# Optimization experiments

Measured on AMD Instinct MI355X. Metric: run time of the kernel, lower is better.

## Reference

```python
import jax, jax.numpy as jnp
import numpy as np
from jax import lax

TAU = 1.0
LAMBDA_CONTRAST = 1.0
GAMMA_ALIGN = 1.0
EPSILON = 0.1
SINKHORN_ITERS = 50
B, V_EN, V_CN, K, H, D = 512, 30000, 20000, 100, 512, 300


def setup_inputs() -> dict:
    key = jax.random.key(0)
    ks = jax.random.split(key, 24)
    s = lambda fan_in: 1.0 / np.sqrt(fan_in)
    inp = {
        'x_bow_en': jax.random.uniform(ks[0], (B, V_EN), jnp.float32),
        'x_bow_cn': jax.random.uniform(ks[1], (B, V_CN), jnp.float32),
        'cluster_ids': jax.random.randint(ks[2], (B,), 0, 9, jnp.int32),
        'eps_en': jax.random.normal(ks[3], (B, K), jnp.float32),
        'eps_cn': jax.random.normal(ks[4], (B, K), jnp.float32),
        # English encoder params
        'W1_en': jax.random.normal(ks[5], (V_EN, H), jnp.float32) * s(V_EN),
        'b1_en': jnp.zeros((H,), jnp.float32),
        'W2_en': jax.random.normal(ks[6], (H, H), jnp.float32) * s(H),
        'b2_en': jnp.zeros((H,), jnp.float32),
        'Wmu_en': jax.random.normal(ks[7], (H, K), jnp.float32) * s(H),
        'bmu_en': jnp.zeros((K,), jnp.float32),
        'Wlv_en': jax.random.normal(ks[8], (H, K), jnp.float32) * s(H),
        'blv_en': jnp.zeros((K,), jnp.float32),
        # Chinese encoder params
        'W1_cn': jax.random.normal(ks[9], (V_CN, H), jnp.float32) * s(V_CN),
        'b1_cn': jnp.zeros((H,), jnp.float32),
        'W2_cn': jax.random.normal(ks[10], (H, H), jnp.float32) * s(H),
        'b2_cn': jnp.zeros((H,), jnp.float32),
        'Wmu_cn': jax.random.normal(ks[11], (H, K), jnp.float32) * s(H),
        'bmu_cn': jnp.zeros((K,), jnp.float32),
        'Wlv_cn': jax.random.normal(ks[12], (H, K), jnp.float32) * s(H),
        'blv_cn': jnp.zeros((K,), jnp.float32),
        # frozen word embeddings + topic embeddings
        'word_emb_en': jax.random.normal(ks[13], (V_EN, D), jnp.float32),
        'word_emb_cn': jax.random.normal(ks[14], (V_CN, D), jnp.float32),
        'topic_emb': jax.random.normal(ks[15], (K, D), jnp.float32),
    }
    return inp


def _encoder(x, eps, W1, b1, W2, b2, Wmu, bmu, Wlv, blv):
    h = jax.nn.softplus(x @ W1 + b1)
    h = jax.nn.softplus(h @ W2 + b2)
    mu = h @ Wmu + bmu
    logvar = h @ Wlv + blv
    z = mu + eps * jnp.exp(0.5 * logvar)  # reparameterization
    theta = jax.nn.softmax(z, axis=-1)
    return theta, mu, logvar


def _compute_beta(word_emb, topic_emb, tau):
    # torch.cdist p=2 -> euclidean distance [V, K]
    sq = (jnp.sum(word_emb ** 2, -1)[:, None] + jnp.sum(topic_emb ** 2, -1)[None, :]
          - 2.0 * word_emb @ topic_emb.T)
    dist = jnp.sqrt(jnp.maximum(sq, 0.0))
    beta = jnp.exp(-dist / tau)
    beta = beta / jnp.sum(beta, axis=0, keepdims=True)  # normalize over vocab
    return beta.T  # [K, V]


def _tm_loss(x_bow, theta, beta, mu, logvar):
    recon = theta @ beta  # [B, V]
    recon_loss = jnp.mean(-jnp.sum(x_bow * jax.nn.log_softmax(recon, axis=-1), axis=-1))
    kl = jnp.mean(0.5 * jnp.sum(jnp.exp(logvar) + mu ** 2 - 1.0 - logvar, axis=-1))
    return recon_loss + kl


def _contrastive_loss(theta_en, theta_cn, cluster_ids, tau):
    b = theta_en.shape[0]
    parity = (jnp.arange(b) % 2 == 0)[:, None]
    thetas = jnp.where(parity, theta_en, theta_cn)  # anchor/other selection
    tn = thetas / jnp.maximum(jnp.linalg.norm(thetas, axis=-1, keepdims=True), 1e-8)
    E = jnp.exp((tn @ tn.T) / tau)  # exp(cos_sim / tau), [B, B]
    offdiag = ~jnp.eye(b, dtype=bool)
    valid = cluster_ids > 0  # falsy cluster -> skipped, matching torch truthiness
    same = cluster_ids[:, None] == cluster_ids[None, :]
    pos_mask = offdiag & same & valid[:, None] & valid[None, :]
    pos_sim = jnp.sum(jnp.where(pos_mask, E, 0.0), axis=1)
    neg_sum = jnp.sum(jnp.where(offdiag, E, 0.0), axis=1)  # all j != i
    has_pos = valid & (jnp.sum(pos_mask, axis=1) > 0)
    per = -jnp.log(pos_sim / (pos_sim + neg_sum + 1e-8))
    loss = jnp.sum(jnp.where(has_pos, per, 0.0))
    count = jnp.sum(has_pos).astype(jnp.float32)
    return loss / (count + 1e-8)


def _sinkhorn(a, b, C, eps):
    Kmat = jnp.exp(-C / eps)
    def step(uv, _):
        u, v = uv
        u = a / (Kmat @ v + 1e-8)
        v = b / (Kmat.T @ u + 1e-8)
        return (u, v), None
    (u, v), _ = lax.scan(step, (jnp.ones_like(a), jnp.ones_like(b)), None, length=SINKHORN_ITERS)
    return u[:, None] * Kmat * v[None, :]


def _alignment_loss(topic_emb, eps):
    tn = topic_emb / jnp.maximum(jnp.linalg.norm(topic_emb, axis=-1, keepdims=True), 1e-8)
    C = 1.0 - tn @ tn.T
    k = topic_emb.shape[0]
    a = jnp.full((k,), 1.0 / k, jnp.float32)
    Q = _sinkhorn(a, a, C, eps)
    return jnp.sum(Q * C)


def reference(x_bow_en, x_bow_cn, cluster_ids, eps_en, eps_cn,
              W1_en, b1_en, W2_en, b2_en, Wmu_en, bmu_en, Wlv_en, blv_en,
              W1_cn, b1_cn, W2_cn, b2_cn, Wmu_cn, bmu_cn, Wlv_cn, blv_cn,
              word_emb_en, word_emb_cn, topic_emb):
    theta_en, mu_en, lv_en = _encoder(x_bow_en, eps_en, W1_en, b1_en, W2_en, b2_en, Wmu_en, bmu_en, Wlv_en, blv_en)
    theta_cn, mu_cn, lv_cn = _encoder(x_bow_cn, eps_cn, W1_cn, b1_cn, W2_cn, b2_cn, Wmu_cn, bmu_cn, Wlv_cn, blv_cn)
    beta_en = _compute_beta(word_emb_en, topic_emb, TAU)
    beta_cn = _compute_beta(word_emb_cn, topic_emb, TAU)
    tm_en = _tm_loss(x_bow_en, theta_en, beta_en, mu_en, lv_en)
    tm_cn = _tm_loss(x_bow_cn, theta_cn, beta_cn, mu_cn, lv_cn)
    contrast = _contrastive_loss(theta_en, theta_cn, cluster_ids, TAU)
    align = _alignment_loss(topic_emb, EPSILON)
    total = tm_en + tm_cn + LAMBDA_CONTRAST * contrast + GAMMA_ALIGN * align
    return total, tm_en, tm_cn, contrast, align, theta_en, theta_cn, beta_en, beta_cn
```

## Files before the change

### kernel.cpp

```cpp
#include <hip/hip_runtime.h>
#include <math.h>

#define BATCH 512
#define VEN 30000
#define VCN 20000
#define KT 100
#define HID 512
#define DIM 300
#define VENP 30080
#define VCNP 20096
#define KDP 320

typedef float f32x4 __attribute__((ext_vector_type(4)));
typedef short bf16x8 __attribute__((ext_vector_type(8)));
typedef unsigned short u16x8 __attribute__((ext_vector_type(8)));
typedef unsigned short u16x4 __attribute__((ext_vector_type(4)));

#define WS_H1_EN   0
#define WS_H2_EN   (WS_H1_EN + 262144)
#define WS_H1_CN   (WS_H2_EN + 262144)
#define WS_H2_CN   (WS_H1_CN + 262144)
#define WS_ROWS_EN (WS_H2_CN + 262144)
#define WS_ROWS_CN (WS_ROWS_EN + 1536)
#define WS_SCAL    (WS_ROWS_CN + 1536)
#define ZERO_FLOATS (WS_SCAL + 64)
#define WS_BIG     ZERO_FLOATS
#define XB_EN      WS_BIG
#define XB_CN      (WS_BIG + 7680000)
#define WEP_EN     WS_BIG
#define WEP_CN     (WS_BIG + 4812800)
#define TEP        (WS_BIG + 4812800 + 3215360)
#define BT_EN      (WS_BIG + 8048640)
#define BT_CN      (BT_EN + 1925120)
#define THP_EN     (BT_CN + 1286144)
#define THP_CN     (THP_EN + 32768)
#define AFTER_BIG  (WS_BIG + 12800000)
#define W1T_EN     AFTER_BIG
#define W1T_CN     (W1T_EN + 7680000)
#define W2T_EN     (W1T_CN + 5120000)
#define W2T_CN     (W2T_EN + 131072)
#define H1B_EN     (W2T_CN + 131072)
#define H1B_CN     (H1B_EN + 131072)
#define WN2_EN     (H1B_CN + 131072)
#define WN2_CN     (WN2_EN + 30080)
#define TN2        (WN2_CN + 20096)
#define WS_TNBUF   (TN2 + 128)
#define WS_TNT     (WS_TNBUF + 51200)
#define WS_CTOP    (WS_TNT + 30000)
#define WS_COLSUM_EN (WS_CTOP + 10000)
#define WS_COLSUM_CN (WS_COLSUM_EN + 128)

#define OUT_THETA_EN 5
#define OUT_THETA_CN (OUT_THETA_EN + 51200)
#define OUT_BETA_EN  (OUT_THETA_CN + 51200)
#define OUT_BETA_CN  (OUT_BETA_EN + 3000000)

__device__ __forceinline__ float waveReduceSum(float v) {
    #pragma unroll
    for (int o = 32; o > 0; o >>= 1) v += __shfl_down(v, o);
    return v;
}

__device__ __forceinline__ unsigned short f2bf(float f) {
    unsigned int u = __float_as_uint(f);
    u = (u + 0x7FFFu + ((u >> 16) & 1u)) >> 16;
    return (unsigned short)u;
}

template <int MODE>
__global__ __launch_bounds__(256)
void mfma_gemm_nt(const unsigned short* __restrict__ A, const unsigned short* __restrict__ B,
                  float* __restrict__ C, int M, int N, int K, int ldA, int ldB, int chunkK,
                  int Mreal, const float* __restrict__ an2, const float* __restrict__ bn2)
{
    __shared__ __align__(16) unsigned short As[128 * 40];
    __shared__ __align__(16) unsigned short Bs[128 * 40];
    const int tid = threadIdx.x;
    const int m0 = blockIdx.x * 128, n0 = blockIdx.y * 128;
    const int kStart = blockIdx.z * chunkK;
    const int kEnd = min(kStart + chunkK, K);

    const int wave = tid >> 6, lane = tid & 63;
    const int wm = (wave & 1) * 64, wn = (wave >> 1) * 64;
    const int l15 = lane & 15, quad = lane >> 4;

    const int srow = tid >> 1;
    const int scol = (tid & 1) * 16;

    f32x4 acc[4][4];
    #pragma unroll
    for (int i = 0; i < 4; ++i)
        #pragma unroll
        for (int j = 0; j < 4; ++j)
            acc[i][j] = (f32x4){0.f, 0.f, 0.f, 0.f};

    const u16x8 z8 = {0,0,0,0,0,0,0,0};

    for (int k0 = kStart; k0 < kEnd; k0 += 32) {
        int kA = k0 + scol;
        {
            const unsigned short* pa = A + (size_t)(m0 + srow) * ldA + kA;
            u16x8 a0 = (kA     < kEnd) ? *(const u16x8*)(pa)     : z8;
            u16x8 a1 = (kA + 8 < kEnd) ? *(const u16x8*)(pa + 8) : z8;
            *(u16x8*)&As[srow * 40 + scol]     = a0;
            *(u16x8*)&As[srow * 40 + scol + 8] = a1;
        }
        {
            const unsigned short* pb = B + (size_t)(n0 + srow) * ldB + kA;
            u16x8 b0 = (kA     < kEnd) ? *(const u16x8*)(pb)     : z8;
            u16x8 b1 = (kA + 8 < kEnd) ? *(const u16x8*)(pb + 8) : z8;
            *(u16x8*)&Bs[srow * 40 + scol]     = b0;
            *(u16x8*)&Bs[srow * 40 + scol + 8] = b1;
        }
        __syncthreads();
        bf16x8 af[4], bfr[4];
        #pragma unroll
        for (int mi = 0; mi < 4; ++mi)
            af[mi] = *(const bf16x8*)&As[(wm + mi * 16 + l15) * 40 + quad * 8];
        #pragma unroll
        for (int ni = 0; ni < 4; ++ni)
            bfr[ni] = *(const bf16x8*)&Bs[(wn + ni * 16 + l15) * 40 + quad * 8];
        #pragma unroll
        for (int mi = 0; mi < 4; ++mi)
            #pragma unroll
            for (int ni = 0; ni < 4; ++ni)
                acc[mi][ni] = __builtin_amdgcn_mfma_f32_16x16x32_bf16(af[mi], bfr[ni], acc[mi][ni], 0, 0, 0);
        __syncthreads();
    }

    if (MODE == 0) {
        #pragma unroll
        for (int mi = 0; mi < 4; ++mi)
            #pragma unroll
            for (int ni = 0; ni < 4; ++ni)
                #pragma unroll
                for (int i = 0; i < 4; ++i) {
                    int m = m0 + wm + mi * 16 + quad * 4 + i;
                    int n = n0 + wn + ni * 16 + l15;
                    atomicAdd(&C[(size_t)m * N + n], acc[mi][ni][i]);
                }
    } else {
        #pragma unroll
        for (int mi = 0; mi < 4; ++mi)
            #pragma unroll
            for (int ni = 0; ni < 4; ++ni)
                #pragma unroll
                for (int i = 0; i < 4; ++i) {
                    int m = m0 + wm + mi * 16 + quad * 4 + i;
                    int n = n0 + wn + ni * 16 + l15;
                    if (m < Mreal && n < KT) {
                        float sq = an2[m] + bn2[n] - 2.f * acc[mi][ni][i];
                        C[(size_t)n * Mreal + m] = __expf(-sqrtf(fmaxf(sq, 0.f)));
                    }
                }
    }
}

__global__ __launch_bounds__(256)
void recon_mfma_kernel(const unsigned short* __restrict__ A, const unsigned short* __restrict__ B,
                       const float* __restrict__ x, int V, float* __restrict__ rows)
{
    __shared__ __align__(16) unsigned short As[128 * 40];
    __shared__ __align__(16) unsigned short Bs[128 * 40];
    const int tid = threadIdx.x;
    const int m0 = blockIdx.x * 128, n0 = blockIdx.y * 128;
    const int wave = tid >> 6, lane = tid & 63;
    const int wm = (wave & 1) * 64, wn = (wave >> 1) * 64;
    const int l15 = lane & 15, quad = lane >> 4;
    const int srow = tid >> 1, scol = (tid & 1) * 16;

    f32x4 acc[4][4];
    #pragma unroll
    for (int i = 0; i < 4; ++i)
        #pragma unroll
        for (int j = 0; j < 4; ++j)
            acc[i][j] = (f32x4){0.f, 0.f, 0.f, 0.f};

    for (int k0 = 0; k0 < 128; k0 += 32) {
        int kA = k0 + scol;
        *(u16x8*)&As[srow * 40 + scol]     = *(const u16x8*)(A + (size_t)(m0 + srow) * 128 + kA);
        *(u16x8*)&As[srow * 40 + scol + 8] = *(const u16x8*)(A + (size_t)(m0 + srow) * 128 + kA + 8);
        *(u16x8*)&Bs[srow * 40 + scol]     = *(const u16x8*)(B + (size_t)(n0 + srow) * 128 + kA);
        *(u16x8*)&Bs[srow * 40 + scol + 8] = *(const u16x8*)(B + (size_t)(n0 + srow) * 128 + kA + 8);
        __syncthreads();
        bf16x8 af[4], bfr[4];
        #pragma unroll
        for (int mi = 0; mi < 4; ++mi)
            af[mi] = *(const bf16x8*)&As[(wm + mi * 16 + l15) * 40 + quad * 8];
        #pragma unroll
        for (int ni = 0; ni < 4; ++ni)
            bfr[ni] = *(const bf16x8*)&Bs[(wn + ni * 16 + l15) * 40 + quad * 8];
        #pragma unroll
        for (int mi = 0; mi < 4; ++mi)
            #pragma unroll
            for (int ni = 0; ni < 4; ++ni)
                acc[mi][ni] = __builtin_amdgcn_mfma_f32_16x16x32_bf16(af[mi], bfr[ni], acc[mi][ni], 0, 0, 0);
        __syncthreads();
    }

    #pragma unroll
    for (int ni = 0; ni < 4; ++ni) {
        int b = n0 + wn + ni * 16 + l15;
        float tse = 0.f, tsxr = 0.f, tsx = 0.f;
        #pragma unroll
        for (int mi = 0; mi < 4; ++mi) {
            int v0 = m0 + wm + mi * 16 + quad * 4;
            if (v0 + 3 < V) {
                float4 xv = *(const float4*)&x[(size_t)b * V + v0];
                float xa[4] = {xv.x, xv.y, xv.z, xv.w};
                #pragma unroll
                for (int i = 0; i < 4; ++i) {
                    float r = acc[mi][ni][i];
                    tse += __expf(r);
                    tsxr += xa[i] * r;
                    tsx  += xa[i];
                }
            } else {
                #pragma unroll
                for (int i = 0; i < 4; ++i) {
                    int v = v0 + i;
                    if (v < V) {
                        float xv1 = x[(size_t)b * V + v];
                        float r = acc[mi][ni][i];
                        tse += __expf(r); tsxr += xv1 * r; tsx += xv1;
                    }
                }
            }
        }
        tse  += __shfl_xor(tse, 16);  tse  += __shfl_xor(tse, 32);
        tsxr += __shfl_xor(tsxr, 16); tsxr += __shfl_xor(tsxr, 32);
        tsx  += __shfl_xor(tsx, 16);  tsx  += __shfl_xor(tsx, 32);
        if (quad == 0) {
            atomicAdd(&rows[b], tse);
            atomicAdd(&rows[512 + b], tsxr);
            atomicAdd(&rows[1024 + b], tsx);
        }
    }
}

__global__ __launch_bounds__(256)
void cast_bf16_kernel(const float* __restrict__ src, unsigned short* __restrict__ dst, int n4)
{
    int i = blockIdx.x * 256 + threadIdx.x;
    if (i < n4) {
        float4 v = reinterpret_cast<const float4*>(src)[i];
        u16x4 o = { f2bf(v.x), f2bf(v.y), f2bf(v.z), f2bf(v.w) };
        *(u16x4*)&dst[i * 4] = o;
    }
}

__global__ __launch_bounds__(256)
void transpose_cast_kernel(const float* __restrict__ src, unsigned short* __restrict__ dst,
                           int K, int N)
{
    __shared__ float tile[32][33];
    int kb = blockIdx.x * 32, nb = blockIdx.y * 32;
    int tx = threadIdx.x & 31, ty4 = threadIdx.x >> 5;
    #pragma unroll
    for (int j = 0; j < 4; ++j) {
        int k = kb + ty4 * 4 + j;
        tile[ty4 * 4 + j][tx] = (k < K) ? src[(size_t)k * N + nb + tx] : 0.f;
    }
    __syncthreads();
    #pragma unroll
    for (int j = 0; j < 4; ++j) {
        int n = nb + ty4 * 4 + j;
        int k = kb + tx;
        if (k < K) dst[(size_t)n * K + k] = f2bf(tile[tx][ty4 * 4 + j]);
    }
}

__global__ void padcast_kernel(const float* __restrict__ src, unsigned short* __restrict__ dst, int V)
{
    int m = blockIdx.x, k = threadIdx.x;
    float v = (m < V && k < DIM) ? src[(size_t)m * DIM + k] : 0.f;
    dst[(size_t)m * KDP + k] = f2bf(v);
}

__global__ __launch_bounds__(256)
void beta_to_bt_kernel(const float* __restrict__ beta, unsigned short* __restrict__ bt,
                       int V)
{
    int v = blockIdx.x * 64 + (threadIdx.x & 63);
    int kq = threadIdx.x >> 6;
    unsigned short tmp[32];
    #pragma unroll
    for (int j = 0; j < 32; ++j) {
        int k = kq * 32 + j;
        float val = (k < KT && v < V) ? beta[(size_t)k * V + v] : 0.f;
        tmp[j] = f2bf(val);
    }
    #pragma unroll
    for (int q = 0; q < 4; ++q)
        *(u16x8*)&bt[(size_t)v * 128 + kq * 32 + q * 8] = *(u16x8*)&tmp[q * 8];
}

__global__ void theta_pad_kernel(const float* __restrict__ theta, unsigned short* __restrict__ thp)
{
    int idx = blockIdx.x * 256 + threadIdx.x;
    int b = idx >> 7, k = idx & 127;
    thp[idx] = f2bf(k < KT ? theta[b * KT + k] : 0.f);
}

__global__ void sqnorm_rows_kernel(const float* __restrict__ A, float* __restrict__ out,
                                   int rows, int cols)
{
    int r = blockIdx.x;
    float s = 0.f;
    for (int d = threadIdx.x; d < cols; d += 64) { float a = A[(size_t)r * cols + d]; s += a * a; }
    s = waveReduceSum(s);
    if (threadIdx.x == 0) out[r] = s;
}

__global__ __launch_bounds__(256)
void colsum_kernel(const float* __restrict__ bta, float* __restrict__ cs, int V)
{
    int k = blockIdx.x, tid = threadIdx.x;
    float s = 0.f;
    for (int v = tid; v < V; v += 256) s += bta[(size_t)k * V + v];
    s = waveReduceSum(s);
    __shared__ float cw[4];
    if ((tid & 63) == 0) cw[tid >> 6] = s;
    __syncthreads();
    if (tid == 0) cs[k] = cw[0] + cw[1] + cw[2] + cw[3];
}

__global__ void normbeta_kernel(float* __restrict__ bta, const float* __restrict__ cs, int V)
{
    int v = blockIdx.x * 256 + threadIdx.x;
    int k = blockIdx.y;
    if (v < V) bta[(size_t)k * V + v] *= (1.0f / cs[k]);
}

__global__ void bias_softplus_bf16_kernel(const float* __restrict__ src, const float* __restrict__ b,
                                          unsigned short* __restrict__ dst, int n)
{
    int i = blockIdx.x * 256 + threadIdx.x;
    if (i < n) {
        float x = src[i] + b[i & (HID - 1)];
        float sp = fmaxf(x, 0.f) + log1pf(__expf(-fabsf(x)));
        dst[i] = f2bf(sp);
    }
}

__global__ void bias_softplus_f32_kernel(float* __restrict__ y, const float* __restrict__ b, int n)
{
    int i = blockIdx.x * 256 + threadIdx.x;
    if (i < n) {
        float x = y[i] + b[i & (HID - 1)];
        y[i] = fmaxf(x, 0.f) + log1pf(__expf(-fabsf(x)));
    }
}

__global__ __launch_bounds__(128)
void encoder_head_kernel(const float* __restrict__ h2, const float* __restrict__ Wmu,
                         const float* __restrict__ bmu, const float* __restrict__ Wlv,
                         const float* __restrict__ blv, const float* __restrict__ eps,
                         float* __restrict__ theta_out, float* __restrict__ kl_accum)
{
    int i = blockIdx.x, tid = threadIdx.x;
    __shared__ float hrow[HID];
    __shared__ float sred[128];
    #pragma unroll
    for (int j = 0; j < 4; ++j) hrow[tid + 128 * j] = h2[i * HID + tid + 128 * j];
    __syncthreads();
    float mu = 0.f, lv = 0.f;
    if (tid < KT) {
        #pragma unroll 8
        for (int h = 0; h < HID; ++h) {
            float hv = hrow[h];
            mu += hv * Wmu[h * KT + tid];
            lv += hv * Wlv[h * KT + tid];
        }
        mu += bmu[tid]; lv += blv[tid];
    }
    float z = (tid < KT) ? (mu + eps[i * KT + tid] * __expf(0.5f * lv)) : -3.0e38f;
    sred[tid] = z; __syncthreads();
    for (int s = 64; s > 0; s >>= 1) { if (tid < s) sred[tid] = fmaxf(sred[tid], sred[tid + s]); __syncthreads(); }
    float zmax = sred[0]; __syncthreads();
    float e = (tid < KT) ? __expf(z - zmax) : 0.f;
    sred[tid] = e; __syncthreads();
    for (int s = 64; s > 0; s >>= 1) { if (tid < s) sred[tid] += sred[tid + s]; __syncthreads(); }
    float esum = sred[0]; __syncthreads();
    if (tid < KT) theta_out[i * KT + tid] = e / esum;
    float kterm = (tid < KT) ? 0.5f * (__expf(lv) + mu * mu - 1.f - lv) : 0.f;
    sred[tid] = kterm; __syncthreads();
    for (int s = 64; s > 0; s >>= 1) { if (tid < s) sred[tid] += sred[tid + s]; __syncthreads(); }
    if (tid == 0) atomicAdd(kl_accum, sred[0]);
}

__global__ __launch_bounds__(256)
void recon_finalize_kernel(const float* __restrict__ rows_en, const float* __restrict__ rows_cn,
                           float* __restrict__ scal)
{
    const float* rows = (blockIdx.x == 0) ? rows_en : rows_cn;
    int tid = threadIdx.x;
    float s = 0.f;
    for (int r = tid; r < 512; r += 256) {
        float se = rows[r], sxr = rows[512 + r], sx = rows[1024 + r];
        s += __logf(se) * sx - sxr;
    }
    s = waveReduceSum(s);
    __shared__ float cw[4];
    if ((tid & 63) == 0) cw[tid >> 6] = s;
    __syncthreads();
    if (tid == 0) scal[5 + blockIdx.x] = cw[0] + cw[1] + cw[2] + cw[3];
}

__global__ __launch_bounds__(128)
void contrast_prep_kernel(const float* __restrict__ theta_en, const float* __restrict__ theta_cn,
                          float* __restrict__ tn)
{
    int i = blockIdx.x, tid = threadIdx.x;
    const float* src = ((i & 1) == 0) ? theta_en : theta_cn;
    float val = (tid < KT) ? src[i * KT + tid] : 0.f;
    __shared__ float sred[128];
    sred[tid] = val * val; __syncthreads();
    for (int s = 64; s > 0; s >>= 1) { if (tid < s) sred[tid] += sred[tid + s]; __syncthreads(); }
    float inv = 1.0f / fmaxf(sqrtf(sred[0]), 1e-8f);
    if (tid < KT) tn[i * KT + tid] = val * inv;
}

__global__ __launch_bounds__(256)
void contrast_main_kernel(const float* __restrict__ tn, const int* __restrict__ cid,
                          float* __restrict__ scal)
{
    int i = blockIdx.x, tid = threadIdx.x;
    __shared__ __align__(16) float ti[KT];
    if (tid < KT) ti[tid] = tn[i * KT + tid];
    __syncthreads();
    int ci = cid[i];
    bool vi = ci > 0;
    float pos = 0.f, neg = 0.f, pcnt = 0.f;
    for (int j = tid; j < 512; j += 256) {
        if (j == i) continue;
        float s = 0.f;
        const float4* tj = reinterpret_cast<const float4*>(&tn[j * KT]);
        #pragma unroll
        for (int q = 0; q < 25; ++q) {
            float4 t4 = tj[q];
            s += ti[4 * q] * t4.x + ti[4 * q + 1] * t4.y + ti[4 * q + 2] * t4.z + ti[4 * q + 3] * t4.w;
        }
        float E = __expf(s);
        neg += E;
        if (vi && cid[j] == ci) { pos += E; pcnt += 1.f; }
    }
    pos = waveReduceSum(pos); neg = waveReduceSum(neg); pcnt = waveReduceSum(pcnt);
    __shared__ float cw[3][4];
    int w = tid >> 6;
    if ((tid & 63) == 0) { cw[0][w] = pos; cw[1][w] = neg; cw[2][w] = pcnt; }
    __syncthreads();
    if (tid == 0) {
        float P = 0.f, N = 0.f, PC = 0.f;
        for (int q = 0; q < 4; ++q) { P += cw[0][q]; N += cw[1][q]; PC += cw[2][q]; }
        if (vi && PC > 0.f) {
            atomicAdd(&scal[2], -__logf(P / (P + N + 1e-8f)));
            atomicAdd(&scal[3], 1.0f);
        }
    }
}

__global__ void norm_rows_kernel(const float* __restrict__ A, float* __restrict__ out, int cols)
{
    int r = blockIdx.x, tid = threadIdx.x;
    float s = 0.f;
    for (int d = tid; d < cols; d += 64) { float a = A[r * cols + d]; s += a * a; }
    s = waveReduceSum(s);
    s = __shfl(s, 0);
    float inv = 1.0f / fmaxf(sqrtf(s), 1e-8f);
    for (int d = tid; d < cols; d += 64) out[r * cols + d] = A[r * cols + d] * inv;
}

__global__ __launch_bounds__(128)
void ctopic_kernel(const float* __restrict__ tnt, float* __restrict__ C)
{
    int i = blockIdx.x, tid = threadIdx.x;
    __shared__ float ti[DIM];
    for (int d = tid; d < DIM; d += 128) ti[d] = tnt[i * DIM + d];
    __syncthreads();
    for (int j = tid; j < KT; j += 128) {
        float s = 0.f;
        for (int d = 0; d < DIM; ++d) s += ti[d] * tnt[j * DIM + d];
        C[i * KT + j] = 1.0f - s;
    }
}

__global__ __launch_bounds__(512)
void sinkhorn_kernel(const float* __restrict__ C, float* __restrict__ scal)
{
    __shared__ float Ks[KT * 101];
    __shared__ float Cs[KT * 101];
    __shared__ float u[KT], v[KT];
    int tid = threadIdx.x;
    for (int t = tid; t < KT * KT; t += 512) {
        int i = t / KT, j = t % KT;
        float c = C[t];
        Cs[i * 101 + j] = c;
        Ks[i * 101 + j] = __expf(-c * 10.0f);
    }
    if (tid < KT) { u[tid] = 1.f; v[tid] = 1.f; }
    __syncthreads();
    int row = tid >> 2, q = tid & 3;
    bool act = tid < 400;
    for (int it = 0; it < 50; ++it) {
        if (act) {
            float s = 0.f;
            for (int j = q * 25; j < q * 25 + 25; ++j) s += Ks[row * 101 + j] * v[j];
            s += __shfl_xor(s, 1); s += __shfl_xor(s, 2);
            if (q == 0) u[row] = 0.01f / (s + 1e-8f);
        }
        __syncthreads();
        if (act) {
            float s = 0.f;
            for (int j = q * 25; j < q * 25 + 25; ++j) s += Ks[j * 101 + row] * u[j];
            s += __shfl_xor(s, 1); s += __shfl_xor(s, 2);
            if (q == 0) v[row] = 0.01f / (s + 1e-8f);
        }
        __syncthreads();
    }
    float part = 0.f;
    for (int t = tid; t < KT * KT; t += 512) {
        int i = t / KT, j = t % KT;
        part += u[i] * Ks[i * 101 + j] * v[j] * Cs[i * 101 + j];
    }
    part = waveReduceSum(part);
    __shared__ float cw[8];
    if ((tid & 63) == 0) cw[tid >> 6] = part;
    __syncthreads();
    if (tid == 0) {
        float s = 0.f;
        for (int w = 0; w < 8; ++w) s += cw[w];
        scal[4] = s;
    }
}

__global__ void final_combine_kernel(const float* __restrict__ scal, float* __restrict__ out)
{
    if (threadIdx.x == 0 && blockIdx.x == 0) {
        const float invB = 1.0f / 512.0f;
        float tm_en = scal[5] * invB + scal[0] * invB;
        float tm_cn = scal[6] * invB + scal[1] * invB;
        float contrast = scal[2] / (scal[3] + 1e-8f);
        float align = scal[4];
        out[0] = tm_en + tm_cn + contrast + align;
        out[1] = tm_en;
        out[2] = tm_cn;
        out[3] = contrast;
        out[4] = align;
    }
}

extern "C" void kernel_launch(void* const* d_in, const int* in_sizes, int n_in,
                              void* d_out_v, int out_size, void* d_ws, size_t ws_size,
                              hipStream_t stream)
{
    const float* x_en   = (const float*)d_in[0];
    const float* x_cn   = (const float*)d_in[1];
    const int*   cid    = (const int*)  d_in[2];
    const float* eps_en = (const float*)d_in[3];
    const float* eps_cn = (const float*)d_in[4];
    const float* W1_en  = (const float*)d_in[5];
    const float* b1_en  = (const float*)d_in[6];
    const float* W2_en  = (const float*)d_in[7];
    const float* b2_en  = (const float*)d_in[8];
    const float* Wmu_en = (const float*)d_in[9];
    const float* bmu_en = (const float*)d_in[10];
    const float* Wlv_en = (const float*)d_in[11];
    const float* blv_en = (const float*)d_in[12];
    const float* W1_cn  = (const float*)d_in[13];
    const float* b1_cn  = (const float*)d_in[14];
    const float* W2_cn  = (const float*)d_in[15];
    const float* b2_cn  = (const float*)d_in[16];
    const float* Wmu_cn = (const float*)d_in[17];
    const float* bmu_cn = (const float*)d_in[18];
    const float* Wlv_cn = (const float*)d_in[19];
    const float* blv_cn = (const float*)d_in[20];
    const float* we_en  = (const float*)d_in[21];
    const float* we_cn  = (const float*)d_in[22];
    const float* te     = (const float*)d_in[23];
    float* out = (float*)d_out_v;
    float* ws  = (float*)d_ws;

    unsigned short* xb_en  = (unsigned short*)(ws + XB_EN);
    unsigned short* xb_cn  = (unsigned short*)(ws + XB_CN);
    unsigned short* w1t_en = (unsigned short*)(ws + W1T_EN);
    unsigned short* w1t_cn = (unsigned short*)(ws + W1T_CN);
    unsigned short* w2t_en = (unsigned short*)(ws + W2T_EN);
    unsigned short* w2t_cn = (unsigned short*)(ws + W2T_CN);
    unsigned short* h1b_en = (unsigned short*)(ws + H1B_EN);
    unsigned short* h1b_cn = (unsigned short*)(ws + H1B_CN);
    unsigned short* wep_en = (unsigned short*)(ws + WEP_EN);
    unsigned short* wep_cn = (unsigned short*)(ws + WEP_CN);
    unsigned short* tep    = (unsigned short*)(ws + TEP);
    unsigned short* bt_en  = (unsigned short*)(ws + BT_EN);
    unsigned short* bt_cn  = (unsigned short*)(ws + BT_CN);
    unsigned short* thp_en = (unsigned short*)(ws + THP_EN);
    unsigned short* thp_cn = (unsigned short*)(ws + THP_CN);

    hipMemsetAsync(d_ws, 0, (size_t)ZERO_FLOATS * sizeof(float), stream);

    cast_bf16_kernel<<<15000, 256, 0, stream>>>(x_en, xb_en, 3840000);
    cast_bf16_kernel<<<10000, 256, 0, stream>>>(x_cn, xb_cn, 2560000);
    transpose_cast_kernel<<<dim3(938, 16), 256, 0, stream>>>(W1_en, w1t_en, VEN, HID);
    transpose_cast_kernel<<<dim3(625, 16), 256, 0, stream>>>(W1_cn, w1t_cn, VCN, HID);
    transpose_cast_kernel<<<dim3(16, 16), 256, 0, stream>>>(W2_en, w2t_en, HID, HID);
    transpose_cast_kernel<<<dim3(16, 16), 256, 0, stream>>>(W2_cn, w2t_cn, HID, HID);

    mfma_gemm_nt<0><<<dim3(4, 4, 32), 256, 0, stream>>>(xb_en, w1t_en, ws + WS_H1_EN,
        BATCH, HID, VEN, VEN, VEN, 960, 0, nullptr, nullptr);
    mfma_gemm_nt<0><<<dim3(4, 4, 32), 256, 0, stream>>>(xb_cn, w1t_cn, ws + WS_H1_CN,
        BATCH, HID, VCN, VCN, VCN, 640, 0, nullptr, nullptr);

    bias_softplus_bf16_kernel<<<1024, 256, 0, stream>>>(ws + WS_H1_EN, b1_en, h1b_en, 262144);
    bias_softplus_bf16_kernel<<<1024, 256, 0, stream>>>(ws + WS_H1_CN, b1_cn, h1b_cn, 262144);

    mfma_gemm_nt<0><<<dim3(4, 4, 8), 256, 0, stream>>>(h1b_en, w2t_en, ws + WS_H2_EN,
        BATCH, HID, HID, HID, HID, 64, 0, nullptr, nullptr);
    mfma_gemm_nt<0><<<dim3(4, 4, 8), 256, 0, stream>>>(h1b_cn, w2t_cn, ws + WS_H2_CN,
        BATCH, HID, HID, HID, HID, 64, 0, nullptr, nullptr);

    bias_softplus_f32_kernel<<<1024, 256, 0, stream>>>(ws + WS_H2_EN, b2_en, 262144);
    bias_softplus_f32_kernel<<<1024, 256, 0, stream>>>(ws + WS_H2_CN, b2_cn, 262144);

    encoder_head_kernel<<<BATCH, 128, 0, stream>>>(ws + WS_H2_EN, Wmu_en, bmu_en, Wlv_en, blv_en,
                                                   eps_en, out + OUT_THETA_EN, ws + WS_SCAL + 0);
    encoder_head_kernel<<<BATCH, 128, 0, stream>>>(ws + WS_H2_CN, Wmu_cn, bmu_cn, Wlv_cn, blv_cn,
                                                   eps_cn, out + OUT_THETA_CN, ws + WS_SCAL + 1);

    padcast_kernel<<<VENP, KDP, 0, stream>>>(we_en, wep_en, VEN);
    padcast_kernel<<<VCNP, KDP, 0, stream>>>(we_cn, wep_cn, VCN);
    padcast_kernel<<<128, KDP, 0, stream>>>(te, tep, KT);
    sqnorm_rows_kernel<<<VEN, 64, 0, stream>>>(we_en, ws + WN2_EN, VEN, DIM);
    sqnorm_rows_kernel<<<VCN, 64, 0, stream>>>(we_cn, ws + WN2_CN, VCN, DIM);
    sqnorm_rows_kernel<<<KT, 64, 0, stream>>>(te, ws + TN2, KT, DIM);

    mfma_gemm_nt<2><<<dim3(235, 1, 1), 256, 0, stream>>>(wep_en, tep, out + OUT_BETA_EN,
        VENP, 128, KDP, KDP, KDP, KDP, VEN, ws + WN2_EN, ws + TN2);
    mfma_gemm_nt<2><<<dim3(157, 1, 1), 256, 0, stream>>>(wep_cn, tep, out + OUT_BETA_CN,
        VCNP, 128, KDP, KDP, KDP, KDP, VCN, ws + WN2_CN, ws + TN2);

    colsum_kernel<<<KT, 256, 0, stream>>>(out + OUT_BETA_EN, ws + WS_COLSUM_EN, VEN);
    colsum_kernel<<<KT, 256, 0, stream>>>(out + OUT_BETA_CN, ws + WS_COLSUM_CN, VCN);
    normbeta_kernel<<<dim3(118, KT), 256, 0, stream>>>(out + OUT_BETA_EN, ws + WS_COLSUM_EN, VEN);
    normbeta_kernel<<<dim3(79, KT), 256, 0, stream>>>(out + OUT_BETA_CN, ws + WS_COLSUM_CN, VCN);

    beta_to_bt_kernel<<<VENP / 64, 256, 0, stream>>>(out + OUT_BETA_EN, bt_en, VEN);
    beta_to_bt_kernel<<<VCNP / 64, 256, 0, stream>>>(out + OUT_BETA_CN, bt_cn, VCN);
    theta_pad_kernel<<<256, 256, 0, stream>>>(out + OUT_THETA_EN, thp_en);
    theta_pad_kernel<<<256, 256, 0, stream>>>(out + OUT_THETA_CN, thp_cn);

    recon_mfma_kernel<<<dim3(VENP / 128, 4), 256, 0, stream>>>(bt_en, thp_en, x_en, VEN, ws + WS_ROWS_EN);
    recon_mfma_kernel<<<dim3(VCNP / 128, 4), 256, 0, stream>>>(bt_cn, thp_cn, x_cn, VCN, ws + WS_ROWS_CN);
    recon_finalize_kernel<<<2, 256, 0, stream>>>(ws + WS_ROWS_EN, ws + WS_ROWS_CN, ws + WS_SCAL);

    contrast_prep_kernel<<<BATCH, 128, 0, stream>>>(out + OUT_THETA_EN, out + OUT_THETA_CN, ws + WS_TNBUF);
    contrast_main_kernel<<<BATCH, 256, 0, stream>>>(ws + WS_TNBUF, cid, ws + WS_SCAL);

    norm_rows_kernel<<<KT, 64, 0, stream>>>(te, ws + WS_TNT, DIM);
    ctopic_kernel<<<KT, 128, 0, stream>>>(ws + WS_TNT, ws + WS_CTOP);
    sinkhorn_kernel<<<1, 512, 0, stream>>>(ws + WS_CTOP, ws + WS_SCAL);

    final_combine_kernel<<<1, 64, 0, stream>>>(ws + WS_SCAL, out);
}
```

Measured before the change: 927.7 us.

## Fuse bf16 casts into GEMM loads, merge padcast/sqnorm and normbeta/bt, register-resident Sinkhorn

The first-layer encoder GEMM now reads the fp32 bag-of-words input directly and converts it to bf16 while staging to LDS, which removes the separate cast kernels and their intermediate buffers. Word-embedding padding and squared-norm computation are merged into one kernel, and beta normalization is merged with the transpose to the bf16 layout, so the large arrays are read fewer times. The Sinkhorn kernel keeps each thread's K row and column in registers with 100 active threads, reducing LDS traffic per iteration. The trade-offs are doubled fp32 A-tile loads inside the GEMM loop, heavy register pressure in the Sinkhorn kernel, and row-strided accesses in the fused beta kernel.

```diff
diff --git a/kernel.cpp b/kernel.cpp
--- a/kernel.cpp
+++ b/kernel.cpp
@@ -25,8 +25,6 @@
 #define WS_SCAL    (WS_ROWS_CN + 1536)
 #define ZERO_FLOATS (WS_SCAL + 64)
 #define WS_BIG     ZERO_FLOATS
-#define XB_EN      WS_BIG
-#define XB_CN      (WS_BIG + 7680000)
 #define WEP_EN     WS_BIG
 #define WEP_CN     (WS_BIG + 4812800)
 #define TEP        (WS_BIG + 4812800 + 3215360)
@@ -67,9 +65,9 @@
     return (unsigned short)u;
 }
 
-template <int MODE>
+template <int MODE, int AF32>
 __global__ __launch_bounds__(256)
-void mfma_gemm_nt(const unsigned short* __restrict__ A, const unsigned short* __restrict__ B,
+void mfma_gemm_nt(const void* __restrict__ Av, const unsigned short* __restrict__ B,
                   float* __restrict__ C, int M, int N, int K, int ldA, int ldB, int chunkK,
                   int Mreal, const float* __restrict__ an2, const float* __restrict__ bn2)
 {
@@ -98,8 +96,23 @@
 
     for (int k0 = kStart; k0 < kEnd; k0 += 32) {
         int kA = k0 + scol;
-        {
-            const unsigned short* pa = A + (size_t)(m0 + srow) * ldA + kA;
+        if (AF32) {
+            const float* pa = (const float*)Av + (size_t)(m0 + srow) * ldA + kA;
+            float4 f0 = {0,0,0,0}, f1 = {0,0,0,0}, f2 = {0,0,0,0}, f3 = {0,0,0,0};
+            if (kA < kEnd) {
+                f0 = *(const float4*)(pa);
+                f1 = *(const float4*)(pa + 4);
+                f2 = *(const float4*)(pa + 8);
+                f3 = *(const float4*)(pa + 12);
+            }
+            u16x8 o0 = { f2bf(f0.x), f2bf(f0.y), f2bf(f0.z), f2bf(f0.w),
+                         f2bf(f1.x), f2bf(f1.y), f2bf(f1.z), f2bf(f1.w) };
+            u16x8 o1 = { f2bf(f2.x), f2bf(f2.y), f2bf(f2.z), f2bf(f2.w),
+                         f2bf(f3.x), f2bf(f3.y), f2bf(f3.z), f2bf(f3.w) };
+            *(u16x8*)&As[srow * 40 + scol]     = o0;
+            *(u16x8*)&As[srow * 40 + scol + 8] = o1;
+        } else {
+            const unsigned short* pa = (const unsigned short*)Av + (size_t)(m0 + srow) * ldA + kA;
             u16x8 a0 = (kA     < kEnd) ? *(const u16x8*)(pa)     : z8;
             u16x8 a1 = (kA + 8 < kEnd) ? *(const u16x8*)(pa + 8) : z8;
             *(u16x8*)&As[srow * 40 + scol]     = a0;
@@ -239,17 +252,6 @@
 }
 
 __global__ __launch_bounds__(256)
-void cast_bf16_kernel(const float* __restrict__ src, unsigned short* __restrict__ dst, int n4)
-{
-    int i = blockIdx.x * 256 + threadIdx.x;
-    if (i < n4) {
-        float4 v = reinterpret_cast<const float4*>(src)[i];
-        u16x4 o = { f2bf(v.x), f2bf(v.y), f2bf(v.z), f2bf(v.w) };
-        *(u16x4*)&dst[i * 4] = o;
-    }
-}
-
-__global__ __launch_bounds__(256)
 void transpose_cast_kernel(const float* __restrict__ src, unsigned short* __restrict__ dst,
                            int K, int N)
 {
@@ -270,16 +272,25 @@
     }
 }
 
-__global__ void padcast_kernel(const float* __restrict__ src, unsigned short* __restrict__ dst, int V)
-{
-    int m = blockIdx.x, k = threadIdx.x;
-    float v = (m < V && k < DIM) ? src[(size_t)m * DIM + k] : 0.f;
-    dst[(size_t)m * KDP + k] = f2bf(v);
+__global__ void padcast_sqnorm_kernel(const float* __restrict__ src, unsigned short* __restrict__ dst,
+                                      float* __restrict__ n2, int V)
+{
+    int m = blockIdx.x, tid = threadIdx.x;
+    float sq = 0.f;
+    #pragma unroll
+    for (int j = 0; j < 5; ++j) {
+        int k = tid + j * 64;
+        float v = (m < V && k < DIM) ? src[(size_t)m * DIM + k] : 0.f;
+        dst[(size_t)m * KDP + k] = f2bf(v);
+        sq += v * v;
+    }
+    sq = waveReduceSum(sq);
+    if (tid == 0) n2[m] = sq;
 }
 
 __global__ __launch_bounds__(256)
-void beta_to_bt_kernel(const float* __restrict__ beta, unsigned short* __restrict__ bt,
-                       int V)
+void normbeta_bt_kernel(float* __restrict__ beta, const float* __restrict__ cs,
+                        unsigned short* __restrict__ bt, int V)
 {
     int v = blockIdx.x * 64 + (threadIdx.x & 63);
     int kq = threadIdx.x >> 6;
@@ -287,7 +298,11 @@
     #pragma unroll
     for (int j = 0; j < 32; ++j) {
         int k = kq * 32 + j;
-        float val = (k < KT && v < V) ? beta[(size_t)k * V + v] : 0.f;
+        float val = 0.f;
+        if (k < KT && v < V) {
+            val = beta[(size_t)k * V + v] * (1.0f / cs[k]);
+            beta[(size_t)k * V + v] = val;
+        }
         tmp[j] = f2bf(val);
     }
     #pragma unroll
@@ -300,16 +315,6 @@
     int idx = blockIdx.x * 256 + threadIdx.x;
     int b = idx >> 7, k = idx & 127;
     thp[idx] = f2bf(k < KT ? theta[b * KT + k] : 0.f);
-}
-
-__global__ void sqnorm_rows_kernel(const float* __restrict__ A, float* __restrict__ out,
-                                   int rows, int cols)
-{
-    int r = blockIdx.x;
-    float s = 0.f;
-    for (int d = threadIdx.x; d < cols; d += 64) { float a = A[(size_t)r * cols + d]; s += a * a; }
-    s = waveReduceSum(s);
-    if (threadIdx.x == 0) out[r] = s;
 }
 
 __global__ __launch_bounds__(256)
@@ -323,13 +328,6 @@
     if ((tid & 63) == 0) cw[tid >> 6] = s;
     __syncthreads();
     if (tid == 0) cs[k] = cw[0] + cw[1] + cw[2] + cw[3];
-}
-
-__global__ void normbeta_kernel(float* __restrict__ bta, const float* __restrict__ cs, int V)
-{
-    int v = blockIdx.x * 256 + threadIdx.x;
-    int k = blockIdx.y;
-    if (v < V) bta[(size_t)k * V + v] *= (1.0f / cs[k]);
 }
 
 __global__ void bias_softplus_bf16_kernel(const float* __restrict__ src, const float* __restrict__ b,
@@ -485,53 +483,70 @@
     }
 }
 
-__global__ __launch_bounds__(512)
+__global__ __launch_bounds__(128, 1)
 void sinkhorn_kernel(const float* __restrict__ C, float* __restrict__ scal)
 {
-    __shared__ float Ks[KT * 101];
-    __shared__ float Cs[KT * 101];
-    __shared__ float u[KT], v[KT];
-    int tid = threadIdx.x;
-    for (int t = tid; t < KT * KT; t += 512) {
-        int i = t / KT, j = t % KT;
-        float c = C[t];
-        Cs[i * 101 + j] = c;
-        Ks[i * 101 + j] = __expf(-c * 10.0f);
-    }
-    if (tid < KT) { u[tid] = 1.f; v[tid] = 1.f; }
-    __syncthreads();
-    int row = tid >> 2, q = tid & 3;
-    bool act = tid < 400;
+    __shared__ __align__(16) float ld[100 * 101];
+    __shared__ __align__(16) float ub[128], vb[128];
+    __shared__ float cw[2];
+    const int tid = threadIdx.x;
+
+    for (int i = tid; i < 10000; i += 128) {
+        int r = i / 100, c = i - r * 100;
+        ld[r * 101 + c] = C[i];
+    }
+    ub[tid] = 1.f; vb[tid] = 1.f;
+    __syncthreads();
+
+    float kr[100], kc[100];
+    if (tid < 100) {
+        #pragma unroll
+        for (int j = 0; j < 100; ++j) kr[j] = __expf(-10.f * ld[tid * 101 + j]);
+        #pragma unroll
+        for (int j = 0; j < 100; ++j) kc[j] = __expf(-10.f * ld[j * 101 + tid]);
+    }
+
     for (int it = 0; it < 50; ++it) {
-        if (act) {
+        if (tid < 100) {
             float s = 0.f;
-            for (int j = q * 25; j < q * 25 + 25; ++j) s += Ks[row * 101 + j] * v[j];
-            s += __shfl_xor(s, 1); s += __shfl_xor(s, 2);
-            if (q == 0) u[row] = 0.01f / (s + 1e-8f);
+            #pragma unroll
+            for (int q = 0; q < 25; ++q) {
+                float4 v4 = *(const float4*)&vb[q * 4];
+                s += kr[q*4]*v4.x + kr[q*4+1]*v4.y + kr[q*4+2]*v4.z + kr[q*4+3]*v4.w;
+            }
+            ub[tid] = 0.01f / (s + 1e-8f);
         }
         __syncthreads();
-        if (act) {
+        if (tid < 100) {
             float s = 0.f;
-            for (int j = q * 25; j < q * 25 + 25; ++j) s += Ks[j * 101 + row] * u[j];
-            s += __shfl_xor(s, 1); s += __shfl_xor(s, 2);
-            if (q == 0) v[row] = 0.01f / (s + 1e-8f);
+            #pragma unroll
+            for (int q = 0; q < 25; ++q) {
+                float4 u4 = *(const float4*)&ub[q * 4];
+                s += kc[q*4]*u4.x + kc[q*4+1]*u4.y + kc[q*4+2]*u4.z + kc[q*4+3]*u4.w;
+            }
+            vb[tid] = 0.01f / (s + 1e-8f);
         }
         __syncthreads();
     }
+
     float part = 0.f;
-    for (int t = tid; t < KT * KT; t += 512) {
-        int i = t / KT, j = t % KT;
-        part += u[i] * Ks[i * 101 + j] * v[j] * Cs[i * 101 + j];
+    if (tid < 100) {
+        float u = ub[tid];
+        #pragma unroll
+        for (int q = 0; q < 25; ++q) {
+            float4 v4 = *(const float4*)&vb[q * 4];
+            float va[4] = {v4.x, v4.y, v4.z, v4.w};
+            #pragma unroll
+            for (int e = 0; e < 4; ++e) {
+                int j = q * 4 + e;
+                part += u * kr[j] * va[e] * ld[tid * 101 + j];
+            }
+        }
     }
     part = waveReduceSum(part);
-    __shared__ float cw[8];
     if ((tid & 63) == 0) cw[tid >> 6] = part;
     __syncthreads();
-    if (tid == 0) {
-        float s = 0.f;
-        for (int w = 0; w < 8; ++w) s += cw[w];
-        scal[4] = s;
-    }
+    if (tid == 0) scal[4] = cw[0] + cw[1];
 }
 
 __global__ void final_combine_kernel(const float* __restrict__ scal, float* __restrict__ out)
@@ -581,8 +596,6 @@
     float* out = (float*)d_out_v;
     float* ws  = (float*)d_ws;
 
-    unsigned short* xb_en  = (unsigned short*)(ws + XB_EN);
-    unsigned short* xb_cn  = (unsigned short*)(ws + XB_CN);
     unsigned short* w1t_en = (unsigned short*)(ws + W1T_EN);
     unsigned short* w1t_cn = (unsigned short*)(ws + W1T_CN);
     unsigned short* w2t_en = (unsigned short*)(ws + W2T_EN);
@@ -599,24 +612,22 @@
 
     hipMemsetAsync(d_ws, 0, (size_t)ZERO_FLOATS * sizeof(float), stream);
 
-    cast_bf16_kernel<<<15000, 256, 0, stream>>>(x_en, xb_en, 3840000);
-    cast_bf16_kernel<<<10000, 256, 0, stream>>>(x_cn, xb_cn, 2560000);
     transpose_cast_kernel<<<dim3(938, 16), 256, 0, stream>>>(W1_en, w1t_en, VEN, HID);
     transpose_cast_kernel<<<dim3(625, 16), 256, 0, stream>>>(W1_cn, w1t_cn, VCN, HID);
     transpose_cast_kernel<<<dim3(16, 16), 256, 0, stream>>>(W2_en, w2t_en, HID, HID);
     transpose_cast_kernel<<<dim3(16, 16), 256, 0, stream>>>(W2_cn, w2t_cn, HID, HID);
 
-    mfma_gemm_nt<0><<<dim3(4, 4, 32), 256, 0, stream>>>(xb_en, w1t_en, ws + WS_H1_EN,
+    mfma_gemm_nt<0, 1><<<dim3(4, 4, 32), 256, 0, stream>>>(x_en, w1t_en, ws + WS_H1_EN,
         BATCH, HID, VEN, VEN, VEN, 960, 0, nullptr, nullptr);
-    mfma_gemm_nt<0><<<dim3(4, 4, 32), 256, 0, stream>>>(xb_cn, w1t_cn, ws + WS_H1_CN,
+    mfma_gemm_nt<0, 1><<<dim3(4, 4, 32), 256, 0, stream>>>(x_cn, w1t_cn, ws + WS_H1_CN,
         BATCH, HID, VCN, VCN, VCN, 640, 0, nullptr, nullptr);
 
     bias_softplus_bf16_kernel<<<1024, 256, 0, stream>>>(ws + WS_H1_EN, b1_en, h1b_en, 262144);
     bias_softplus_bf16_kernel<<<1024, 256, 0, stream>>>(ws + WS_H1_CN, b1_cn, h1b_cn, 262144);
 
-    mfma_gemm_nt<0><<<dim3(4, 4, 8), 256, 0, stream>>>(h1b_en, w2t_en, ws + WS_H2_EN,
+    mfma_gemm_nt<0, 0><<<dim3(4, 4, 8), 256, 0, stream>>>(h1b_en, w2t_en, ws + WS_H2_EN,
         BATCH, HID, HID, HID, HID, 64, 0, nullptr, nullptr);
-    mfma_gemm_nt<0><<<dim3(4, 4, 8), 256, 0, stream>>>(h1b_cn, w2t_cn, ws + WS_H2_CN,
+    mfma_gemm_nt<0, 0><<<dim3(4, 4, 8), 256, 0, stream>>>(h1b_cn, w2t_cn, ws + WS_H2_CN,
         BATCH, HID, HID, HID, HID, 64, 0, nullptr, nullptr);
 
     bias_softplus_f32_kernel<<<1024, 256, 0, stream>>>(ws + WS_H2_EN, b2_en, 262144);
@@ -627,25 +638,21 @@
     encoder_head_kernel<<<BATCH, 128, 0, stream>>>(ws + WS_H2_CN, Wmu_cn, bmu_cn, Wlv_cn, blv_cn,
                                                    eps_cn, out + OUT_THETA_CN, ws + WS_SCAL + 1);
 
-    padcast_kernel<<<VENP, KDP, 0, stream>>>(we_en, wep_en, VEN);
-    padcast_kernel<<<VCNP, KDP, 0, stream>>>(we_cn, wep_cn, VCN);
-    padcast_kernel<<<128, KDP, 0, stream>>>(te, tep, KT);
-    sqnorm_rows_kernel<<<VEN, 64, 0, stream>>>(we_en, ws + WN2_EN, VEN, DIM);
-    sqnorm_rows_kernel<<<VCN, 64, 0, stream>>>(we_cn, ws + WN2_CN, VCN, DIM);
-    sqnorm_rows_kernel<<<KT, 64, 0, stream>>>(te, ws + TN2, KT, DIM);
-
-    mfma_gemm_nt<2><<<dim3(235, 1, 1), 256, 0, stream>>>(wep_en, tep, out + OUT_BETA_EN,
+    padcast_sqnorm_kernel<<<VENP, 64, 0, stream>>>(we_en, wep_en, ws + WN2_EN, VEN);
+    padcast_sqnorm_kernel<<<VCNP, 64, 0, stream>>>(we_cn, wep_cn, ws + WN2_CN, VCN);
+    padcast_sqnorm_kernel<<<128, 64, 0, stream>>>(te, tep, ws + TN2, KT);
+
+    mfma_gemm_nt<2, 0><<<dim3(235, 1, 1), 256, 0, stream>>>(wep_en, tep, out + OUT_BETA_EN,
         VENP, 128, KDP, KDP, KDP, KDP, VEN, ws + WN2_EN, ws + TN2);
-    mfma_gemm_nt<2><<<dim3(157, 1, 1), 256, 0, stream>>>(wep_cn, tep, out + OUT_BETA_CN,
+    mfma_gemm_nt<2, 0><<<dim3(157, 1, 1), 256, 0, stream>>>(wep_cn, tep, out + OUT_BETA_CN,
         VCNP, 128, KDP, KDP, KDP, KDP, VCN, ws + WN2_CN, ws + TN2);
 
     colsum_kernel<<<KT, 256, 0, stream>>>(out + OUT_BETA_EN, ws + WS_COLSUM_EN, VEN);
     colsum_kernel<<<KT, 256, 0, stream>>>(out + OUT_BETA_CN, ws + WS_COLSUM_CN, VCN);
-    normbeta_kernel<<<dim3(118, KT), 256, 0, stream>>>(out + OUT_BETA_EN, ws + WS_COLSUM_EN, VEN);
-    normbeta_kernel<<<dim3(79, KT), 256, 0, stream>>>(out + OUT_BETA_CN, ws + WS_COLSUM_CN, VCN);
-
-    beta_to_bt_kernel<<<VENP / 64, 256, 0, stream>>>(out + OUT_BETA_EN, bt_en, VEN);
-    beta_to_bt_kernel<<<VCNP / 64, 256, 0, stream>>>(out + OUT_BETA_CN, bt_cn, VCN);
+
+    normbeta_bt_kernel<<<VENP / 64, 256, 0, stream>>>(out + OUT_BETA_EN, ws + WS_COLSUM_EN, bt_en, VEN);
+    normbeta_bt_kernel<<<VCNP / 64, 256, 0, stream>>>(out + OUT_BETA_CN, ws + WS_COLSUM_CN, bt_cn, VCN);
+
     theta_pad_kernel<<<256, 256, 0, stream>>>(out + OUT_THETA_EN, thp_en);
     theta_pad_kernel<<<256, 256, 0, stream>>>(out + OUT_THETA_CN, thp_cn);
 
@@ -658,7 +665,7 @@
 
     norm_rows_kernel<<<KT, 64, 0, stream>>>(te, ws + WS_TNT, DIM);
     ctopic_kernel<<<KT, 128, 0, stream>>>(ws + WS_TNT, ws + WS_CTOP);
-    sinkhorn_kernel<<<1, 512, 0, stream>>>(ws + WS_CTOP, ws + WS_SCAL);
+    sinkhorn_kernel<<<1, 128, 0, stream>>>(ws + WS_CTOP, ws + WS_SCAL);
 
     final_combine_kernel<<<1, 64, 0, stream>>>(ws + WS_SCAL, out);
 }
```

Result: faster. 880.1 us (-5.1%).
